# Performance work log

Hardware: AMD Instinct MI355X
Metric: run time of the kernel (lower is better)

## Reference

```python
import jax, jax.numpy as jnp
import numpy as np

D_MODEL = 1024
N_HEADS = 16
HEAD_DIM = D_MODEL // N_HEADS
NUM_SINK = 4
WINDOW = 512
B, S = 1, 4096


def _sink_visible(S):
    # visible[i, j] = (j <= i) & ((j < NUM_SINK) | (j >= i - WINDOW + 1))
    i = jnp.arange(S)[:, None]
    j = jnp.arange(S)[None, :]
    return (j <= i) & ((j < NUM_SINK) | (j >= i - WINDOW + 1))


def setup_inputs() -> dict:
    key = jax.random.key(0)
    kx, kq, kk, kv, ko = jax.random.split(key, 5)
    sc = 1.0 / np.sqrt(D_MODEL)
    return {
        "x": jax.random.normal(kx, (B, S, D_MODEL), dtype=jnp.float32),
        "Wq": jax.random.normal(kq, (D_MODEL, D_MODEL), dtype=jnp.float32) * sc,
        "Wk": jax.random.normal(kk, (D_MODEL, D_MODEL), dtype=jnp.float32) * sc,
        "Wv": jax.random.normal(kv, (D_MODEL, D_MODEL), dtype=jnp.float32) * sc,
        "Wo": jax.random.normal(ko, (D_MODEL, D_MODEL), dtype=jnp.float32) * sc,
    }


def reference(x, Wq, Wk, Wv, Wo):
    Bx, Sx, D = x.shape
    H, hd = N_HEADS, HEAD_DIM
    # nn.Linear (no bias): y = x @ W^T
    q = (x @ Wq.T).reshape(Bx, Sx, H, hd).transpose(0, 2, 1, 3)  # (B,H,S,hd)
    k = (x @ Wk.T).reshape(Bx, Sx, H, hd).transpose(0, 2, 1, 3)
    v = (x @ Wv.T).reshape(Bx, Sx, H, hd).transpose(0, 2, 1, 3)
    scale = 1.0 / np.sqrt(hd)
    scores = jnp.einsum("bhqd,bhkd->bhqk", q, k) * scale  # (B,H,S,S)
    visible = _sink_visible(Sx)  # (S,S) bool; every row has j=i visible
    scores = jnp.where(visible[None, None], scores, -jnp.inf)
    attn = jax.nn.softmax(scores, axis=-1)
    out = jnp.einsum("bhqk,bhkd->bhqd", attn, v)
    out = out.transpose(0, 2, 1, 3).reshape(Bx, Sx, D)
    return out @ Wo.T
```

## Files before the change

### kernel.cpp

```cpp
#include <hip/hip_runtime.h>
#include <stdint.h>

#define AS1 __attribute__((address_space(1)))
#define AS3 __attribute__((address_space(3)))

typedef short short8 __attribute__((ext_vector_type(8)));
typedef unsigned short ushort8 __attribute__((ext_vector_type(8)));
typedef __bf16 bf16x8 __attribute__((ext_vector_type(8)));
typedef float floatx4 __attribute__((ext_vector_type(4)));

__device__ __forceinline__ floatx4 mfma16(short8 a, short8 b, floatx4 c) {
  return __builtin_amdgcn_mfma_f32_16x16x32_bf16(
      __builtin_bit_cast(bf16x8, a), __builtin_bit_cast(bf16x8, b), c, 0, 0, 0);
}

__device__ __forceinline__ unsigned short f2bf(float f) {
  uint32_t u = __builtin_bit_cast(uint32_t, f);
  u = (u + 0x7FFFu + ((u >> 16) & 1u)) >> 16;
  return (unsigned short)u;
}

__device__ __forceinline__ uint32_t cvt_pk_bf16(float a, float b) {
  uint32_t d;
  asm("v_cvt_pk_bf16_f32 %0, %1, %2" : "=v"(d) : "v"(a), "v"(b));
  return d;
}

__device__ __forceinline__ size_t tiled_off(int row, int col) {
  int rt = row >> 7, c8 = (row >> 4) & 7, rr = row & 15;
  int t = col >> 5, lh = (col >> 3) & 3, e = col & 7;
  return ((size_t)((rt * 32 + t) * 8 + c8) << 9) + (lh * 16 + rr) * 8 + e;
}

__global__ __launch_bounds__(256) void convert_pack(
    const float4* __restrict__ x, const float4* __restrict__ wq,
    const float4* __restrict__ wk, const float4* __restrict__ wv,
    const float4* __restrict__ wo, unsigned short* __restrict__ xb,
    unsigned short* __restrict__ wqkvb, unsigned short* __restrict__ wob) {
  int i = blockIdx.x * 256 + threadIdx.x;
  const float4* src;
  unsigned short* dstbase;
  int row, cb;
  if (i < (1 << 19)) {
    row = i >> 7;
    cb = i & 127;
    src = x + row * 256 + cb * 2;
    dstbase = xb + tiled_off(row, cb * 8);
  } else if (i < 917504) {
    int j = i - (1 << 19);
    int r = j >> 17;
    int jj = j & 131071;
    int rw = jj >> 7;
    cb = jj & 127;
    src = (r == 0 ? wq : r == 1 ? wk : wv) + rw * 256 + cb * 2;
    row = r * 1024 + rw;
    dstbase = wqkvb + tiled_off(row, cb * 8);
  } else {
    int j = i - 917504;
    row = j >> 7;
    cb = j & 127;
    src = wo + row * 256 + cb * 2;
    dstbase = wob + tiled_off(row, cb * 8);
  }
  float4 a = src[0], b = src[1];
  ushort8 o;
  o[0] = f2bf(a.x); o[1] = f2bf(a.y); o[2] = f2bf(a.z); o[3] = f2bf(a.w);
  o[4] = f2bf(b.x); o[5] = f2bf(b.y); o[6] = f2bf(b.z); o[7] = f2bf(b.w);
  *(ushort8*)dstbase = o;
}

template <typename OutT>
__global__ __launch_bounds__(256) void gemm_bt(const unsigned short* __restrict__ A,
                                               const unsigned short* __restrict__ Bm,
                                               OutT* __restrict__ C, int N, int K) {
  __shared__ unsigned short lds[3][16 * 512];
  const int tid = threadIdx.x;
  const int lane = tid & 63;
  const int w = tid >> 6;
  const int wr = w >> 1, wc = w & 1;

  const int lid = blockIdx.y * gridDim.x + blockIdx.x;
  const int xcd = lid & 7;
  const int wgid = xcd * 96 + (lid >> 3);
  const int s = wgid >> 5, w5 = wgid & 31;
  const int mt = (s & 3) * 8 + (w5 & 7);
  const int nt = (s >> 2) * 4 + (w5 >> 3);
  const int tm = mt * 128, tn = nt * 128;
  const int lrow = lane & 15;

  floatx4 acc[4][4];
#pragma unroll
  for (int i = 0; i < 4; ++i)
#pragma unroll
    for (int j = 0; j < 4; ++j) acc[i][j] = floatx4{0.f, 0.f, 0.f, 0.f};

  auto stage = [&](unsigned short* buf, int t) {
#pragma unroll
    for (int c = w * 4; c < w * 4 + 4; ++c) {
      const unsigned short* g;
      if (c < 8)
        g = A + ((size_t)((mt * 32 + t) * 8 + c) << 9) + lane * 8;
      else
        g = Bm + ((size_t)((nt * 32 + t) * 8 + (c - 8)) << 9) + lane * 8;
      __builtin_amdgcn_global_load_lds((const AS1 uint32_t*)g,
                                       (AS3 uint32_t*)(buf + c * 512), 16, 0, 0);
    }
  };

  auto compute = [&](const unsigned short* L) {
    short8 af[4], bf[4];
#pragma unroll
    for (int i = 0; i < 4; ++i)
      af[i] = *(const short8*)&L[(wr * 4 + i) * 512 + lane * 8];
#pragma unroll
    for (int j = 0; j < 4; ++j)
      bf[j] = *(const short8*)&L[(8 + wc * 4 + j) * 512 + lane * 8];
#pragma unroll
    for (int i = 0; i < 4; ++i)
#pragma unroll
      for (int j = 0; j < 4; ++j) acc[i][j] = mfma16(af[i], bf[j], acc[i][j]);
  };

  stage(lds[0], 0);
  stage(lds[1], 1);

  const int T = K >> 5;
  int bt = 0;
  for (int t = 0; t < T - 1; ++t) {
    asm volatile("s_waitcnt vmcnt(4)" ::: "memory");
    __builtin_amdgcn_sched_barrier(0);
    __builtin_amdgcn_s_barrier();
    __builtin_amdgcn_sched_barrier(0);
    if (t + 2 < T) {
      int b2 = (bt + 2 >= 3) ? bt - 1 : bt + 2;
      stage(lds[b2], t + 2);
    }
    compute(lds[bt]);
    bt = (bt + 1 == 3) ? 0 : bt + 1;
  }
  asm volatile("s_waitcnt vmcnt(0)" ::: "memory");
  __builtin_amdgcn_sched_barrier(0);
  __builtin_amdgcn_s_barrier();
  __builtin_amdgcn_sched_barrier(0);
  compute(lds[bt]);

  const int r0 = (lane >> 4) * 4;
#pragma unroll
  for (int i = 0; i < 4; ++i)
#pragma unroll
    for (int j = 0; j < 4; ++j)
#pragma unroll
      for (int r = 0; r < 4; ++r) {
        int row = tm + wr * 64 + i * 16 + r0 + r;
        int col = tn + wc * 64 + j * 16 + lrow;
        float v = acc[i][j][r];
        if constexpr (sizeof(OutT) == 2)
          C[(size_t)row * N + col] = f2bf(v);
        else
          C[(size_t)row * N + col] = v;
      }
}

__global__ __launch_bounds__(256) void gemm64(const unsigned short* __restrict__ A,
                                              const unsigned short* __restrict__ Bm,
                                              float* __restrict__ C, int N, int K) {
  __shared__ unsigned short lds[3][12 * 512];
  const int tid = threadIdx.x;
  const int lane = tid & 63;
  const int w = tid >> 6;
  const int wr = w >> 1, wc = w & 1;

  const int lid = blockIdx.y * gridDim.x + blockIdx.x;
  const int xcd = lid & 7;
  const int wgid = xcd * 64 + (lid >> 3);
  const int s = wgid >> 5, w5 = wgid & 31;
  const int mt = (s & 3) * 16 + (w5 & 15);
  const int nt = (s >> 2) * 2 + (w5 >> 4);
  const int tm = mt * 64, tn = nt * 128;
  const int lrow = lane & 15;
  const int lk = (lane >> 4) * 8;

  floatx4 acc[2][4];
#pragma unroll
  for (int i = 0; i < 2; ++i)
#pragma unroll
    for (int j = 0; j < 4; ++j) acc[i][j] = floatx4{0.f, 0.f, 0.f, 0.f};

  auto stage = [&](unsigned short* buf, int t) {
#pragma unroll
    for (int c = w * 3; c < w * 3 + 3; ++c) {
      const unsigned short* g;
      if (c < 4) {
        g = A + (size_t)(tm + c * 16 + lrow) * K + (t * 32 + lk);
      } else {
        g = Bm + ((size_t)((nt * 32 + t) * 8 + (c - 4)) << 9) + lane * 8;
      }
      __builtin_amdgcn_global_load_lds((const AS1 uint32_t*)g,
                                       (AS3 uint32_t*)(buf + c * 512), 16, 0, 0);
    }
  };

  auto compute = [&](const unsigned short* L) {
    short8 af[2], bf[4];
#pragma unroll
    for (int i = 0; i < 2; ++i)
      af[i] = *(const short8*)&L[(wr * 2 + i) * 512 + lane * 8];
#pragma unroll
    for (int j = 0; j < 4; ++j)
      bf[j] = *(const short8*)&L[(4 + wc * 4 + j) * 512 + lane * 8];
#pragma unroll
    for (int i = 0; i < 2; ++i)
#pragma unroll
      for (int j = 0; j < 4; ++j) acc[i][j] = mfma16(af[i], bf[j], acc[i][j]);
  };

  stage(lds[0], 0);
  stage(lds[1], 1);

  const int T = K >> 5;
  int bt = 0;
  for (int t = 0; t < T - 1; ++t) {
    asm volatile("s_waitcnt vmcnt(3)" ::: "memory");
    __builtin_amdgcn_sched_barrier(0);
    __builtin_amdgcn_s_barrier();
    __builtin_amdgcn_sched_barrier(0);
    if (t + 2 < T) {
      int b2 = (bt + 2 >= 3) ? bt - 1 : bt + 2;
      stage(lds[b2], t + 2);
    }
    compute(lds[bt]);
    bt = (bt + 1 == 3) ? 0 : bt + 1;
  }
  asm volatile("s_waitcnt vmcnt(0)" ::: "memory");
  __builtin_amdgcn_sched_barrier(0);
  __builtin_amdgcn_s_barrier();
  __builtin_amdgcn_sched_barrier(0);
  compute(lds[bt]);

  const int r0 = (lane >> 4) * 4;
#pragma unroll
  for (int i = 0; i < 2; ++i)
#pragma unroll
    for (int j = 0; j < 4; ++j)
#pragma unroll
      for (int r = 0; r < 4; ++r) {
        int row = tm + (wr * 2 + i) * 16 + r0 + r;
        int col = tn + (wc * 4 + j) * 16 + lrow;
        C[(size_t)row * N + col] = acc[i][j][r];
      }
}

__global__ __launch_bounds__(256) void attn_kernel(const unsigned short* __restrict__ qkv,
                                                   unsigned short* __restrict__ aout) {
  __shared__ unsigned short Klds[2][16 * 512];
  __shared__ unsigned short VT[64 * 136];
  __shared__ unsigned short PT[4][16 * 136];

  const int tid = threadIdx.x;
  const int lane = tid & 63;
  const int w = tid >> 6;
  const int lrow = lane & 15;
  const int lkg = lane >> 4;

  const int i = blockIdx.x;
  const int half = i >> 8;
  const int j = (i >> 3) & 31;
  const int h = 2 * (i & 7) + half;
  const int qb = half ? (31 - j) : j;
  const int q0 = qb * 128;

  short8 qf[2][2];
#pragma unroll
  for (int qt = 0; qt < 2; ++qt)
#pragma unroll
    for (int ks = 0; ks < 2; ++ks)
      qf[qt][ks] = *(const short8*)&qkv[(size_t)(q0 + qt * 64 + w * 16 + lrow) * 3072 +
                                        h * 64 + ks * 32 + lkg * 8];

  float m_i[2], l_i[2];
  floatx4 o[4][2];
#pragma unroll
  for (int qt = 0; qt < 2; ++qt) {
    m_i[qt] = -1e30f;
    l_i[qt] = 0.f;
#pragma unroll
    for (int nt = 0; nt < 4; ++nt) o[nt][qt] = floatx4{0.f, 0.f, 0.f, 0.f};
  }

  const float scale2 = 0.125f * 1.44269504088896f;

  if (w < 2) {
    const unsigned short* g = &qkv[(size_t)lrow * 3072 + 1024 + h * 64 + w * 32 + lkg * 8];
    __builtin_amdgcn_global_load_lds((const AS1 uint32_t*)g,
                                     (AS3 uint32_t*)(&Klds[0][w * 512]), 16, 0, 0);
  }
  {
    if (lane < 16) {
      const unsigned short* g0 = &qkv[(size_t)(2 * lane) * 3072 + 2048 + h * 64 + w * 16];
      ushort8 a0 = *(const ushort8*)g0;
      ushort8 a1 = *(const ushort8*)(g0 + 8);
      ushort8 b0 = *(const ushort8*)(g0 + 3072);
      ushort8 b1 = *(const ushort8*)(g0 + 3080);
      uint32_t* vt = (uint32_t*)VT;
#pragma unroll
      for (int dd = 0; dd < 8; ++dd) {
        vt[(w * 16 + dd) * 68 + lane] = (uint32_t)a0[dd] | ((uint32_t)b0[dd] << 16);
        vt[(w * 16 + 8 + dd) * 68 + lane] = (uint32_t)a1[dd] | ((uint32_t)b1[dd] << 16);
      }
    }
  }
  const int kb0 = (q0 - 511 < 16) ? 16 : (q0 - 511);
#pragma unroll
  for (int c = 0; c < 4; ++c) {
    int ch = w * 4 + c;
    int kt = ch >> 1, ks = ch & 1;
    const unsigned short* g =
        &qkv[(size_t)(kb0 + kt * 16 + lrow) * 3072 + 1024 + h * 64 + ks * 32 + lkg * 8];
    __builtin_amdgcn_global_load_lds((const AS1 uint32_t*)g,
                                     (AS3 uint32_t*)(&Klds[1][ch * 512]), 16, 0, 0);
  }
  ushort8 va0, va1, vb0, vb1;
  {
    const unsigned short* g0 = &qkv[(size_t)(kb0 + 2 * lane) * 3072 + 2048 + h * 64 + w * 16];
    va0 = *(const ushort8*)g0;
    va1 = *(const ushort8*)(g0 + 8);
    vb0 = *(const ushort8*)(g0 + 3072);
    vb1 = *(const ushort8*)(g0 + 3080);
  }
  __syncthreads();

#pragma unroll
  for (int qt = 0; qt < 2; ++qt) {
    const int qq = q0 + qt * 64 + w * 16 + lrow;
    floatx4 s0 = floatx4{0.f, 0.f, 0.f, 0.f};
#pragma unroll
    for (int ks = 0; ks < 2; ++ks) {
      short8 kf = *(const short8*)&Klds[0][ks * 512 + lane * 8];
      s0 = mfma16(kf, qf[qt][ks], s0);
    }
    float mx = -1e30f;
    float sv[4];
#pragma unroll
    for (int r = 0; r < 4; ++r) {
      int key = lkg * 4 + r;
      bool vis = (key <= qq) && ((key < 4) || (key >= qq - 511));
      sv[r] = vis ? s0[r] * scale2 : -1e30f;
      mx = fmaxf(mx, sv[r]);
    }
    mx = fmaxf(mx, __shfl_xor(mx, 16));
    mx = fmaxf(mx, __shfl_xor(mx, 32));
    m_i[qt] = mx;
    float p0 = exp2f(sv[0] - mx), p1 = exp2f(sv[1] - mx);
    float p2 = exp2f(sv[2] - mx), p3 = exp2f(sv[3] - mx);
    float ps = (p0 + p1) + (p2 + p3);
    *(uint2*)&PT[w][lrow * 136 + lkg * 4] = uint2{cvt_pk_bf16(p0, p1), cvt_pk_bf16(p2, p3)};
    *(uint2*)&PT[w][lrow * 136 + 16 + lkg * 4] = uint2{0u, 0u};
    ps += __shfl_xor(ps, 16);
    ps += __shfl_xor(ps, 32);
    l_i[qt] = ps;
    short8 pf = *(const short8*)&PT[w][lrow * 136 + lkg * 8];
#pragma unroll
    for (int nt = 0; nt < 4; ++nt) {
      short8 vf = *(const short8*)&VT[(nt * 16 + lrow) * 136 + lkg * 8];
      o[nt][qt] = mfma16(vf, pf, o[nt][qt]);
    }
  }

  int nbuf = 1;
  for (int kb = kb0; kb < q0 + 128; kb += 128) {
    const bool hasnext = (kb + 128 < q0 + 128);
    __syncthreads();
    {
      uint32_t* vt = (uint32_t*)VT;
#pragma unroll
      for (int dd = 0; dd < 8; ++dd) {
        vt[(w * 16 + dd) * 68 + lane] = (uint32_t)va0[dd] | ((uint32_t)vb0[dd] << 16);
        vt[(w * 16 + 8 + dd) * 68 + lane] = (uint32_t)va1[dd] | ((uint32_t)vb1[dd] << 16);
      }
    }
    __syncthreads();

    if (hasnext) {
      const int kn = kb + 128;
#pragma unroll
      for (int c = 0; c < 4; ++c) {
        int ch = w * 4 + c;
        int kt = ch >> 1, ks = ch & 1;
        const unsigned short* g =
            &qkv[(size_t)(kn + kt * 16 + lrow) * 3072 + 1024 + h * 64 + ks * 32 + lkg * 8];
        __builtin_amdgcn_global_load_lds((const AS1 uint32_t*)g,
                                         (AS3 uint32_t*)(&Klds[1 - nbuf][ch * 512]), 16, 0, 0);
      }
      const unsigned short* g0 = &qkv[(size_t)(kn + 2 * lane) * 3072 + 2048 + h * 64 + w * 16];
      va0 = *(const ushort8*)g0;
      va1 = *(const ushort8*)(g0 + 8);
      vb0 = *(const ushort8*)(g0 + 3072);
      vb1 = *(const ushort8*)(g0 + 3080);
    }

#pragma unroll
    for (int qt = 0; qt < 2; ++qt) {
      const int qaT = q0 + qt * 64 + w * 16;
      const int qq = qaT + lrow;
      floatx4 s[8];
#pragma unroll
      for (int ct = 0; ct < 8; ++ct) {
        s[ct] = floatx4{0.f, 0.f, 0.f, 0.f};
#pragma unroll
        for (int ks = 0; ks < 2; ++ks) {
          short8 kf = *(const short8*)&Klds[nbuf][(ct * 2 + ks) * 512 + lane * 8];
          s[ct] = mfma16(kf, qf[qt][ks], s[ct]);
        }
      }
      const bool full = (kb + 127 <= qaT) && (kb >= qaT + 15 - 511);
      float mx = -1e30f;
#pragma unroll
      for (int ct = 0; ct < 8; ++ct)
#pragma unroll
        for (int r = 0; r < 4; ++r) {
          float val = s[ct][r] * scale2;
          if (!full) {
            int key = kb + ct * 16 + lkg * 4 + r;
            bool vis = (key <= qq) && (key >= qq - 511);
            val = vis ? val : -1e30f;
          }
          s[ct][r] = val;
          mx = fmaxf(mx, val);
        }
      mx = fmaxf(mx, __shfl_xor(mx, 16));
      mx = fmaxf(mx, __shfl_xor(mx, 32));
      float nm = fmaxf(m_i[qt], mx);
      float alpha = exp2f(m_i[qt] - nm);
      m_i[qt] = nm;

      float ps = 0.f;
#pragma unroll
      for (int ct = 0; ct < 8; ++ct) {
        float p0 = exp2f(s[ct][0] - nm), p1 = exp2f(s[ct][1] - nm);
        float p2 = exp2f(s[ct][2] - nm), p3 = exp2f(s[ct][3] - nm);
        ps += (p0 + p1) + (p2 + p3);
        *(uint2*)&PT[w][lrow * 136 + ct * 16 + lkg * 4] =
            uint2{cvt_pk_bf16(p0, p1), cvt_pk_bf16(p2, p3)};
      }
      ps += __shfl_xor(ps, 16);
      ps += __shfl_xor(ps, 32);
      l_i[qt] = l_i[qt] * alpha + ps;

#pragma unroll
      for (int nt = 0; nt < 4; ++nt)
#pragma unroll
        for (int r = 0; r < 4; ++r) o[nt][qt][r] *= alpha;

#pragma unroll
      for (int kk = 0; kk < 4; ++kk) {
        short8 pf = *(const short8*)&PT[w][lrow * 136 + kk * 32 + lkg * 8];
#pragma unroll
        for (int nt = 0; nt < 4; ++nt) {
          short8 vf = *(const short8*)&VT[(nt * 16 + lrow) * 136 + kk * 32 + lkg * 8];
          o[nt][qt] = mfma16(vf, pf, o[nt][qt]);
        }
      }
    }
    nbuf ^= 1;
  }

#pragma unroll
  for (int qt = 0; qt < 2; ++qt) {
    const int qq = q0 + qt * 64 + w * 16 + lrow;
    const float inv = 1.0f / l_i[qt];
#pragma unroll
    for (int nt = 0; nt < 4; ++nt) {
      floatx4 ov = o[nt][qt];
      uint32_t lo = cvt_pk_bf16(ov[0] * inv, ov[1] * inv);
      uint32_t hi = cvt_pk_bf16(ov[2] * inv, ov[3] * inv);
      *(uint2*)&aout[(size_t)qq * 1024 + h * 64 + nt * 16 + lkg * 4] = uint2{lo, hi};
    }
  }
}

extern "C" void kernel_launch(void* const* d_in, const int* in_sizes, int n_in,
                              void* d_out, int out_size, void* d_ws, size_t ws_size,
                              hipStream_t stream) {
  const float* x = (const float*)d_in[0];
  const float* wq = (const float*)d_in[1];
  const float* wk = (const float*)d_in[2];
  const float* wv = (const float*)d_in[3];
  const float* wo = (const float*)d_in[4];

  char* ws = (char*)d_ws;
  unsigned short* Xb = (unsigned short*)(ws);
  unsigned short* Wqkv = (unsigned short*)(ws + (8u << 20));
  unsigned short* Wob = (unsigned short*)(ws + (14u << 20));
  unsigned short* QKV = (unsigned short*)(ws + (16u << 20));
  unsigned short* AO = (unsigned short*)(ws + (40u << 20));

  convert_pack<<<4096, 256, 0, stream>>>((const float4*)x, (const float4*)wq,
                                         (const float4*)wk, (const float4*)wv,
                                         (const float4*)wo, Xb, Wqkv, Wob);
  gemm_bt<unsigned short><<<dim3(32, 24), 256, 0, stream>>>(Xb, Wqkv, QKV, 3072, 1024);
  attn_kernel<<<512, 256, 0, stream>>>(QKV, AO);
  gemm64<<<dim3(64, 8), 256, 0, stream>>>(AO, Wob, (float*)d_out, 1024, 1024);
}
```

Measured before the change: 171.8 us.

## Write attention output in tiled layout and make convert_pack write-coalesced

The attention kernel now writes its bf16 output in the same 512-element tiled layout used by the packed weights. The output-projection GEMM can then stage A tiles with fully contiguous 1 KB global_load_lds chunks instead of strided row reads. convert_pack is reorganized so each wavefront produces one contiguous 512-element tile, making its stores contiguous while its loads become 16-row strided. The scattered 8-byte stores from the attention epilogue may cost a little more in exchange.

```diff
diff --git a/kernel.cpp b/kernel.cpp
--- a/kernel.cpp
+++ b/kernel.cpp
@@ -33,40 +33,42 @@
 }
 
 __global__ __launch_bounds__(256) void convert_pack(
-    const float4* __restrict__ x, const float4* __restrict__ wq,
-    const float4* __restrict__ wk, const float4* __restrict__ wv,
-    const float4* __restrict__ wo, unsigned short* __restrict__ xb,
+    const float* __restrict__ x, const float* __restrict__ wq,
+    const float* __restrict__ wk, const float* __restrict__ wv,
+    const float* __restrict__ wo, unsigned short* __restrict__ xb,
     unsigned short* __restrict__ wqkvb, unsigned short* __restrict__ wob) {
-  int i = blockIdx.x * 256 + threadIdx.x;
-  const float4* src;
-  unsigned short* dstbase;
-  int row, cb;
-  if (i < (1 << 19)) {
-    row = i >> 7;
-    cb = i & 127;
-    src = x + row * 256 + cb * 2;
-    dstbase = xb + tiled_off(row, cb * 8);
-  } else if (i < 917504) {
-    int j = i - (1 << 19);
-    int r = j >> 17;
-    int jj = j & 131071;
-    int rw = jj >> 7;
-    cb = jj & 127;
-    src = (r == 0 ? wq : r == 1 ? wk : wv) + rw * 256 + cb * 2;
-    row = r * 1024 + rw;
-    dstbase = wqkvb + tiled_off(row, cb * 8);
+  const int lane = threadIdx.x & 63;
+  const int wid = threadIdx.x >> 6;
+  const int b = blockIdx.x * 4 + wid;
+  const int lrow = lane & 15, lkg = lane >> 4;
+  const float* src;
+  unsigned short* dst;
+  if (b < 8192) {
+    int rt = b >> 8, wi = b & 255, t = wi >> 3, c8 = wi & 7;
+    int row = rt * 128 + c8 * 16 + lrow;
+    src = x + (size_t)row * 1024 + t * 32 + lkg * 8;
+    dst = xb + ((size_t)b << 9) + lane * 8;
+  } else if (b < 14336) {
+    int jb = b - 8192;
+    int rt = jb >> 8, wi = jb & 255, t = wi >> 3, c8 = wi & 7;
+    int row = rt * 128 + c8 * 16 + lrow;
+    int r = row >> 10, srow = row & 1023;
+    const float* m = (r == 0) ? wq : (r == 1) ? wk : wv;
+    src = m + (size_t)srow * 1024 + t * 32 + lkg * 8;
+    dst = wqkvb + ((size_t)jb << 9) + lane * 8;
   } else {
-    int j = i - 917504;
-    row = j >> 7;
-    cb = j & 127;
-    src = wo + row * 256 + cb * 2;
-    dstbase = wob + tiled_off(row, cb * 8);
-  }
-  float4 a = src[0], b = src[1];
+    int jb = b - 14336;
+    int rt = jb >> 8, wi = jb & 255, t = wi >> 3, c8 = wi & 7;
+    int row = rt * 128 + c8 * 16 + lrow;
+    src = wo + (size_t)row * 1024 + t * 32 + lkg * 8;
+    dst = wob + ((size_t)jb << 9) + lane * 8;
+  }
+  float4 a = *(const float4*)src;
+  float4 c = *(const float4*)(src + 4);
   ushort8 o;
   o[0] = f2bf(a.x); o[1] = f2bf(a.y); o[2] = f2bf(a.z); o[3] = f2bf(a.w);
-  o[4] = f2bf(b.x); o[5] = f2bf(b.y); o[6] = f2bf(b.z); o[7] = f2bf(b.w);
-  *(ushort8*)dstbase = o;
+  o[4] = f2bf(c.x); o[5] = f2bf(c.y); o[6] = f2bf(c.z); o[7] = f2bf(c.w);
+  *(ushort8*)dst = o;
 }
 
 template <typename OutT>
@@ -178,7 +180,6 @@
   const int nt = (s >> 2) * 2 + (w5 >> 4);
   const int tm = mt * 64, tn = nt * 128;
   const int lrow = lane & 15;
-  const int lk = (lane >> 4) * 8;
 
   floatx4 acc[2][4];
 #pragma unroll
@@ -190,11 +191,10 @@
 #pragma unroll
     for (int c = w * 3; c < w * 3 + 3; ++c) {
       const unsigned short* g;
-      if (c < 4) {
-        g = A + (size_t)(tm + c * 16 + lrow) * K + (t * 32 + lk);
-      } else {
+      if (c < 4)
+        g = A + ((size_t)(((mt >> 1) * 32 + t) * 8 + ((mt & 1) * 4 + c)) << 9) + lane * 8;
+      else
         g = Bm + ((size_t)((nt * 32 + t) * 8 + (c - 4)) << 9) + lane * 8;
-      }
       __builtin_amdgcn_global_load_lds((const AS1 uint32_t*)g,
                                        (AS3 uint32_t*)(buf + c * 512), 16, 0, 0);
     }
@@ -473,7 +473,8 @@
       floatx4 ov = o[nt][qt];
       uint32_t lo = cvt_pk_bf16(ov[0] * inv, ov[1] * inv);
       uint32_t hi = cvt_pk_bf16(ov[2] * inv, ov[3] * inv);
-      *(uint2*)&aout[(size_t)qq * 1024 + h * 64 + nt * 16 + lkg * 4] = uint2{lo, hi};
+      int col = h * 64 + nt * 16 + lkg * 4;
+      *(uint2*)&aout[tiled_off(qq, col)] = uint2{lo, hi};
     }
   }
 }
@@ -494,9 +495,7 @@
   unsigned short* QKV = (unsigned short*)(ws + (16u << 20));
   unsigned short* AO = (unsigned short*)(ws + (40u << 20));
 
-  convert_pack<<<4096, 256, 0, stream>>>((const float4*)x, (const float4*)wq,
-                                         (const float4*)wk, (const float4*)wv,
-                                         (const float4*)wo, Xb, Wqkv, Wob);
+  convert_pack<<<4096, 256, 0, stream>>>(x, wq, wk, wv, wo, Xb, Wqkv, Wob);
   gemm_bt<unsigned short><<<dim3(32, 24), 256, 0, stream>>>(Xb, Wqkv, QKV, 3072, 1024);
   attn_kernel<<<512, 256, 0, stream>>>(QKV, AO);
   gemm64<<<dim3(64, 8), 256, 0, stream>>>(AO, Wob, (float*)d_out, 1024, 1024);
```

Result: faster. 161.3 us, median of 2 (-6.1%).
